# Kernel optimization log

Measured on AMD Instinct MI355X. Metric: run time of the kernel, lower is better.

Reference implementation:

```python
import jax, jax.numpy as jnp
import numpy as np
import math

B, S, D_MODEL, H = 2, 2048, 1024, 16
HD = D_MODEL // H  # head_dim = 64


def _rope(x, seq_len):
    # x: [B, S, H, HD]; standard rotate-half RoPE with base 10000
    d = x.shape[-1]
    inv_freq = 1.0 / (10000.0 ** (jnp.arange(0, d, 2, dtype=jnp.float32) / d))
    t = jnp.arange(seq_len, dtype=jnp.float32)
    freqs = t[:, None] * inv_freq[None, :]              # [S, HD/2]
    emb = jnp.concatenate([freqs, freqs], axis=-1)      # [S, HD]
    cos = jnp.cos(emb)[None, :, None, :]
    sin = jnp.sin(emb)[None, :, None, :]
    x1, x2 = jnp.split(x, 2, axis=-1)
    rot = jnp.concatenate([-x2, x1], axis=-1)
    return x * cos + rot * sin


def setup_inputs() -> dict:
    key = jax.random.key(0)
    ks = jax.random.split(key, 11)
    s = 1.0 / math.sqrt(D_MODEL)
    return {
        "query": jax.random.normal(ks[0], (B, S, D_MODEL), jnp.float32),
        "keys": jax.random.normal(ks[1], (B, S, D_MODEL), jnp.float32),
        "values": jax.random.normal(ks[2], (B, S, D_MODEL), jnp.float32),
        "Wq": jax.random.normal(ks[3], (D_MODEL, D_MODEL), jnp.float32) * s,
        "bq": jnp.zeros((D_MODEL,), jnp.float32),
        "Wk": jax.random.normal(ks[4], (D_MODEL, D_MODEL), jnp.float32) * s,
        "bk": jnp.zeros((D_MODEL,), jnp.float32),
        "Wv": jax.random.normal(ks[5], (D_MODEL, D_MODEL), jnp.float32) * s,
        "bv": jnp.zeros((D_MODEL,), jnp.float32),
        "Wo": jax.random.normal(ks[6], (D_MODEL, D_MODEL), jnp.float32) * s,
        "bo": jnp.zeros((D_MODEL,), jnp.float32),
    }


def reference(query, keys, values, Wq, bq, Wk, bk, Wv, bv, Wo, bo):
    b, s, _ = query.shape
    scale = math.sqrt(HD)
    q = (query @ Wq.T + bq).reshape(b, s, H, HD)   # [B,S,H,HD]
    k = (keys @ Wk.T + bk).reshape(b, s, H, HD)
    v = (values @ Wv.T + bv).reshape(b, s, H, HD)
    q = _rope(q, s)
    k = _rope(k, s)
    # scores: [B,H,Sq,Sk]
    scores = jnp.einsum('bqhd,bkhd->bhqk', q, k)
    causal = jnp.tril(jnp.ones((s, s), dtype=bool))[None, None]
    scores = jnp.where(causal, scores, -jnp.inf) / scale
    attn = jax.nn.softmax(scores, axis=-1)
    ctx = jnp.einsum('bhqk,bkhd->bqhd', attn, v).reshape(b, s, H * HD)
    out = ctx @ Wo.T + bo
    return out, attn
```

## Files before the change

kernel.cpp:

```cpp
#include <hip/hip_runtime.h>
#include <hip/hip_bf16.h>
#include <stdint.h>
#include <math.h>


typedef __attribute__((ext_vector_type(8))) __bf16 bf16x8;
typedef __attribute__((ext_vector_type(4))) float f32x4;

__device__ __forceinline__ unsigned short f2bf(float f) {
  unsigned int u = __float_as_uint(f);
  u += 0x7fffu + ((u >> 16) & 1u);
  return (unsigned short)(u >> 16);
}

typedef const __attribute__((address_space(1))) unsigned int* gas_ptr;
typedef __attribute__((address_space(3))) unsigned int* las_ptr;
__device__ __forceinline__ void glds16(const void* g, void* l) {
  __builtin_amdgcn_global_load_lds((gas_ptr)g, (las_ptr)l, 16, 0, 0);
}

__global__ __launch_bounds__(256) void cvt_all(
    const float* __restrict__ a0, const float* __restrict__ a1,
    const float* __restrict__ a2, const float* __restrict__ w0,
    const float* __restrict__ w1, const float* __restrict__ w2,
    const float* __restrict__ w3, unsigned short* __restrict__ ws,
    float2* __restrict__ rtab) {
  const int z = blockIdx.z;
  if (z == 7) {
    const int i = blockIdx.x * 256 + threadIdx.x;
    if (i < 65536) {
      const int spos = i >> 5, d = i & 31;
      const double invf = pow(10000.0, -(double)d / 32.0);
      double sn, cs;
      sincos((double)spos * invf, &sn, &cs);
      rtab[i] = make_float2((float)cs, (float)sn);
    }
    return;
  }
  const float* src;
  unsigned short* dst;
  int n;
  if (z == 0)      { src = a0; dst = ws;             n = 4194304; }
  else if (z == 1) { src = a1; dst = ws + 4194304;   n = 4194304; }
  else if (z == 2) { src = a2; dst = ws + 8388608;   n = 4194304; }
  else if (z == 3) { src = w0; dst = ws + 12582912;  n = 1048576; }
  else if (z == 4) { src = w1; dst = ws + 13631488;  n = 1048576; }
  else if (z == 5) { src = w2; dst = ws + 14680064;  n = 1048576; }
  else             { src = w3; dst = ws + 15728640;  n = 1048576; }
  const int n4 = n >> 2;
  for (int i = blockIdx.x * 256 + threadIdx.x; i < n4; i += gridDim.x * 256) {
    float4 f = ((const float4*)src)[i];
    ushort4 u;
    u.x = f2bf(f.x); u.y = f2bf(f.y); u.z = f2bf(f.z); u.w = f2bf(f.w);
    ((ushort4*)dst)[i] = u;
  }
}

__global__ __launch_bounds__(256) void gemm_qkv(
    const unsigned short* __restrict__ xq, const unsigned short* __restrict__ xk,
    const unsigned short* __restrict__ xv, const unsigned short* __restrict__ wq,
    const unsigned short* __restrict__ wk, const unsigned short* __restrict__ wv,
    const float* __restrict__ bq, const float* __restrict__ bk,
    const float* __restrict__ bv, const float2* __restrict__ rtab,
    unsigned short* __restrict__ qo, unsigned short* __restrict__ ko,
    unsigned short* __restrict__ vo) {
  const int z = blockIdx.z;
  const unsigned short* A = (z == 0) ? xq : (z == 1) ? xk : xv;
  const unsigned short* W = (z == 0) ? wq : (z == 1) ? wk : wv;
  const float* bias = (z == 0) ? bq : (z == 1) ? bk : bv;
  unsigned short* out = (z == 0) ? qo : (z == 1) ? ko : vo;

  const int t = threadIdx.x;
  const int lane = t & 63, wave = t >> 6;
  const int wr = wave >> 1, wc = wave & 1;
  const int lrow = lane & 15, lkb = lane >> 4;
  const int lin = blockIdx.x + (blockIdx.y << 3);
  const int nl = ((lin & 7) << 5) | (lin >> 3);
  const int m0 = (nl >> 3) * 128, n0 = (nl & 7) * 128;

  __shared__ __align__(16) unsigned short abuf[8192];
  __shared__ __align__(16) unsigned short bbuf[8192];

  f32x4 acc[4][4] = {};

  for (int k0 = 0; k0 < 1024; k0 += 64) {
    __syncthreads();
#pragma unroll
    for (int i = 0; i < 4; ++i) {
      int slot = i * 256 + t;
      int kb = slot >> 7, row = slot & 127;
      glds16(A + (size_t)(m0 + row) * 1024 + k0 + kb * 8, &abuf[slot * 8]);
      glds16(W + (size_t)(n0 + row) * 1024 + k0 + kb * 8, &bbuf[slot * 8]);
    }
    __syncthreads();
#pragma unroll
    for (int ks = 0; ks < 2; ++ks) {
      bf16x8 af[4], bfr[4];
#pragma unroll
      for (int mi = 0; mi < 4; ++mi)
        af[mi] = *(const bf16x8*)&abuf[((ks * 4 + lkb) * 128 + wr * 64 + mi * 16 + lrow) * 8];
#pragma unroll
      for (int ni = 0; ni < 4; ++ni)
        bfr[ni] = *(const bf16x8*)&bbuf[((ks * 4 + lkb) * 128 + wc * 64 + ni * 16 + lrow) * 8];
#pragma unroll
      for (int mi = 0; mi < 4; ++mi)
#pragma unroll
        for (int ni = 0; ni < 4; ++ni)
          acc[mi][ni] = __builtin_amdgcn_mfma_f32_16x16x32_bf16(af[mi], bfr[ni],
                                                                acc[mi][ni], 0, 0, 0);
    }
  }

  const int nbase = n0 + wc * 64;
  float bias_v[4];
#pragma unroll
  for (int ni = 0; ni < 4; ++ni) bias_v[ni] = bias[nbase + ni * 16 + lrow];

  const int mbase = m0 + wr * 64 + 4 * lkb;
  const bool rope = (z < 2);
  const float qsc = (z == 0) ? 0.125f : 1.0f;

#pragma unroll
  for (int mi = 0; mi < 4; ++mi) {
#pragma unroll
    for (int r = 0; r < 4; ++r) {
      const int m = mbase + mi * 16 + r;
      const int bidx = m >> 11, spos = m & 2047;
      float vals[4];
#pragma unroll
      for (int ni = 0; ni < 4; ++ni) vals[ni] = acc[mi][ni][r] + bias_v[ni];
      if (rope) {
#pragma unroll
        for (int ni = 0; ni < 2; ++ni) {
          const int d = ni * 16 + lrow;
          const float2 cs2 = rtab[spos * 32 + d];
          float x1 = vals[ni], x2 = vals[ni + 2];
          vals[ni] = (x1 * cs2.x - x2 * cs2.y) * qsc;
          vals[ni + 2] = (x2 * cs2.x + x1 * cs2.y) * qsc;
        }
      }
#pragma unroll
      for (int ni = 0; ni < 4; ++ni) {
        const int n = nbase + ni * 16 + lrow;
        const int h = n >> 6, d = n & 63;
        out[(size_t)((bidx * 16 + h) * 2048 + spos) * 64 + d] = f2bf(vals[ni]);
      }
    }
  }
}

__global__ __launch_bounds__(256) void gemm_out(
    const unsigned short* __restrict__ A, const unsigned short* __restrict__ W,
    const float* __restrict__ bias, float* __restrict__ out) {
  const int t = threadIdx.x;
  const int lane = t & 63, wave = t >> 6;
  const int wr = wave >> 1, wc = wave & 1;
  const int lrow = lane & 15, lkb = lane >> 4;
  const int lin = blockIdx.x + (blockIdx.y << 3);
  const int nl = ((lin & 7) << 5) | (lin >> 3);
  const int m0 = (nl >> 3) * 128, n0 = (nl & 7) * 128;

  __shared__ __align__(16) unsigned short abuf[8192];
  __shared__ __align__(16) unsigned short bbuf[8192];

  f32x4 acc[4][4] = {};

  for (int k0 = 0; k0 < 1024; k0 += 64) {
    __syncthreads();
#pragma unroll
    for (int i = 0; i < 4; ++i) {
      int slot = i * 256 + t;
      int kb = slot >> 7, row = slot & 127;
      glds16(A + (size_t)(m0 + row) * 1024 + k0 + kb * 8, &abuf[slot * 8]);
      glds16(W + (size_t)(n0 + row) * 1024 + k0 + kb * 8, &bbuf[slot * 8]);
    }
    __syncthreads();
#pragma unroll
    for (int ks = 0; ks < 2; ++ks) {
      bf16x8 af[4], bfr[4];
#pragma unroll
      for (int mi = 0; mi < 4; ++mi)
        af[mi] = *(const bf16x8*)&abuf[((ks * 4 + lkb) * 128 + wr * 64 + mi * 16 + lrow) * 8];
#pragma unroll
      for (int ni = 0; ni < 4; ++ni)
        bfr[ni] = *(const bf16x8*)&bbuf[((ks * 4 + lkb) * 128 + wc * 64 + ni * 16 + lrow) * 8];
#pragma unroll
      for (int mi = 0; mi < 4; ++mi)
#pragma unroll
        for (int ni = 0; ni < 4; ++ni)
          acc[mi][ni] = __builtin_amdgcn_mfma_f32_16x16x32_bf16(af[mi], bfr[ni],
                                                                acc[mi][ni], 0, 0, 0);
    }
  }

  const int nbase = n0 + wc * 64;
  float bias_v[4];
#pragma unroll
  for (int ni = 0; ni < 4; ++ni) bias_v[ni] = bias[nbase + ni * 16 + lrow];
  const int mbase = m0 + wr * 64 + 4 * lkb;
#pragma unroll
  for (int mi = 0; mi < 4; ++mi)
#pragma unroll
    for (int r = 0; r < 4; ++r) {
      const int m = mbase + mi * 16 + r;
      float* orow = out + (size_t)m * 1024 + nbase;
#pragma unroll
      for (int ni = 0; ni < 4; ++ni)
        orow[ni * 16 + lrow] = acc[mi][ni][r] + bias_v[ni];
    }
}

__global__ __launch_bounds__(256) void transpose_v(
    const unsigned short* __restrict__ v, unsigned short* __restrict__ vt) {
  const int s0 = blockIdx.x * 64;
  const int bh = blockIdx.y;
  __shared__ __align__(16) unsigned short tile[64][80];
  const int t = threadIdx.x;
  {
    const int row = t >> 2, cb = t & 3;
    const unsigned short* src = v + (size_t)(bh * 2048 + s0 + row) * 64 + cb * 16;
    *(uint4*)&tile[row][cb * 16] = *(const uint4*)src;
    *(uint4*)&tile[row][cb * 16 + 8] = *(const uint4*)(src + 8);
  }
  __syncthreads();
  {
    const int d = t >> 2, sc = t & 3;
    __align__(16) unsigned short tmp[16];
#pragma unroll
    for (int u = 0; u < 16; ++u) tmp[u] = tile[sc * 16 + u][d];
    unsigned short* dst = vt + (size_t)(bh * 64 + d) * 2048 + s0 + sc * 16;
    *(uint4*)dst = *(const uint4*)&tmp[0];
    *(uint4*)(dst + 8) = *(const uint4*)&tmp[8];
  }
}

__global__ __launch_bounds__(256) void attn_kernel(
    const unsigned short* __restrict__ Q, const unsigned short* __restrict__ Km,
    const unsigned short* __restrict__ Vt, float* __restrict__ attn,
    unsigned short* __restrict__ ctx) {
  const int p = blockIdx.x;
  const int qta = p, qtb = 31 - p;
  const int bh = blockIdx.y;
  const int t = threadIdx.x;
  const int lane = t & 63, wave = t >> 6;
  const int lrow = lane & 15, lg = lane >> 4;
  const int wq0a = qta * 64 + wave * 16;
  const int wq0b = qtb * 64 + wave * 16;

  const unsigned short* Qb = Q + (size_t)bh * 2048 * 64;
  const unsigned short* Kb = Km + (size_t)bh * 2048 * 64;
  const unsigned short* Vb = Vt + (size_t)bh * 64 * 2048;
  float* attn_b = attn + (size_t)bh * 2048 * 2048;

  __shared__ __align__(16) unsigned short kbuf[4096];
  __shared__ __align__(16) unsigned short vbuf[4096];
  __shared__ __align__(16) unsigned short pbuf[4][1024];

  bf16x8 qfa[2], qfb[2];
#pragma unroll
  for (int dk = 0; dk < 2; ++dk) {
    qfa[dk] = *(const bf16x8*)(Qb + (size_t)(wq0a + lrow) * 64 + dk * 32 + lg * 8);
    qfb[dk] = *(const bf16x8*)(Qb + (size_t)(wq0b + lrow) * 64 + dk * 32 + lg * 8);
  }

  float l_a[4] = {0.f, 0.f, 0.f, 0.f};
  float l_b[4] = {0.f, 0.f, 0.f, 0.f};

  auto lupdate = [&](const unsigned short* buf, int kbase, int wq0,
                     const bf16x8* qf, float* l_loc) {
    f32x4 s[4] = {};
#pragma unroll
    for (int fc = 0; fc < 4; ++fc)
#pragma unroll
      for (int dk = 0; dk < 2; ++dk) {
        bf16x8 kf = *(const bf16x8*)&buf[((dk * 4 + lg) * 64 + fc * 16 + lrow) * 8];
        s[fc] = __builtin_amdgcn_mfma_f32_16x16x32_bf16(qf[dk], kf, s[fc], 0, 0, 0);
      }
#pragma unroll
    for (int r = 0; r < 4; ++r) {
      const int qg = wq0 + 4 * lg + r;
      float sum = 0.f;
#pragma unroll
      for (int fc = 0; fc < 4; ++fc) {
        const int kg = kbase + fc * 16 + lrow;
        sum += __expf((kg <= qg) ? s[fc][r] : -1e30f);
      }
      l_loc[r] += sum;
    }
  };

  for (int kt = 0; kt <= qtb; kt += 2) {
    const int k0 = kt * 64;
    const bool two = (kt + 1) <= qtb;
    __syncthreads();
#pragma unroll
    for (int i = 0; i < 2; ++i) {
      int slot = i * 256 + t;
      int cb = slot >> 6, row = slot & 63;
      glds16(Kb + (size_t)(k0 + row) * 64 + cb * 8, &kbuf[slot * 8]);
      if (two)
        glds16(Kb + (size_t)(k0 + 64 + row) * 64 + cb * 8, &vbuf[slot * 8]);
    }
    __syncthreads();
    if (kt <= qta) lupdate(kbuf, k0, wq0a, qfa, l_a);
    lupdate(kbuf, k0, wq0b, qfb, l_b);
    if (two) {
      if (kt + 1 <= qta) lupdate(vbuf, k0 + 64, wq0a, qfa, l_a);
      lupdate(vbuf, k0 + 64, wq0b, qfb, l_b);
    }
  }

  float loglinva[4], loglinvb[4];
#pragma unroll
  for (int r = 0; r < 4; ++r) {
    float la = l_a[r], lb = l_b[r];
#pragma unroll
    for (int off = 1; off < 16; off <<= 1) {
      la += __shfl_xor(la, off);
      lb += __shfl_xor(lb, off);
    }
    loglinva[r] = -__logf(la);
    loglinvb[r] = -__logf(lb);
  }

  f32x4 oaa[4] = {};
  f32x4 oab[4] = {};

  auto process = [&](int k0, int wq0, const bf16x8* qf, const float* loglinv,
                     f32x4* oa) {
    f32x4 s[4] = {};
#pragma unroll
    for (int fc = 0; fc < 4; ++fc)
#pragma unroll
      for (int dk = 0; dk < 2; ++dk) {
        bf16x8 kf = *(const bf16x8*)&kbuf[((dk * 4 + lg) * 64 + fc * 16 + lrow) * 8];
        s[fc] = __builtin_amdgcn_mfma_f32_16x16x32_bf16(qf[dk], kf, s[fc], 0, 0, 0);
      }
#pragma unroll
    for (int r = 0; r < 4; ++r) {
      const int qg = wq0 + 4 * lg + r;
      const int q_ = 4 * lg + r;
      float* arow = attn_b + (size_t)qg * 2048 + k0;
#pragma unroll
      for (int fc = 0; fc < 4; ++fc) {
        const int kg = k0 + fc * 16 + lrow;
        const float pv = (kg <= qg) ? __expf(s[fc][r] + loglinv[r]) : 0.f;
        arow[fc * 16 + lrow] = pv;
        const int k_ = fc * 16 + lrow;
        const int dl = q_ + 16 * ((k_ >> 3) & 3);
        const int kk = k_ >> 5, j = k_ & 7;
        int byteo = (kk * 64 + dl) * 16 + j * 2;
        byteo ^= ((kk * 8 + (dl >> 3)) & 7) << 4;
        *(unsigned short*)((char*)pbuf[wave] + byteo) = f2bf(pv);
      }
    }
#pragma unroll
    for (int kk = 0; kk < 2; ++kk) {
      int rbyte = (kk * 64 + lane) * 16;
      rbyte ^= ((kk * 8 + (lane >> 3)) & 7) << 4;
      bf16x8 pa = *(const bf16x8*)((char*)pbuf[wave] + rbyte);
#pragma unroll
      for (int fd = 0; fd < 4; ++fd) {
        bf16x8 vf = *(const bf16x8*)&vbuf[((kk * 4 + lg) * 64 + fd * 16 + lrow) * 8];
        oa[fd] = __builtin_amdgcn_mfma_f32_16x16x32_bf16(pa, vf, oa[fd], 0, 0, 0);
      }
    }
  };

  for (int kt = 0; kt <= qtb; ++kt) {
    const int k0 = kt * 64;
    __syncthreads();
#pragma unroll
    for (int i = 0; i < 2; ++i) {
      int slot = i * 256 + t;
      int cb = slot >> 6, row = slot & 63;
      glds16(Kb + (size_t)(k0 + row) * 64 + cb * 8, &kbuf[slot * 8]);
      glds16(Vb + (size_t)row * 2048 + k0 + cb * 8, &vbuf[slot * 8]);
    }
    __syncthreads();
    if (kt <= qta) process(k0, wq0a, qfa, loglinva, oaa);
    process(k0, wq0b, qfb, loglinvb, oab);
  }

  {
    const int zc0a = (qta + 1) * 16;
    for (int rr = 0; rr < 16; ++rr) {
      float4* arow = (float4*)(attn_b + (size_t)(wq0a + rr) * 2048);
      for (int c = zc0a + lane; c < 512; c += 64)
        arow[c] = make_float4(0.f, 0.f, 0.f, 0.f);
    }
    const int zc0b = (qtb + 1) * 16;
    for (int rr = 0; rr < 16; ++rr) {
      float4* arow = (float4*)(attn_b + (size_t)(wq0b + rr) * 2048);
      for (int c = zc0b + lane; c < 512; c += 64)
        arow[c] = make_float4(0.f, 0.f, 0.f, 0.f);
    }
  }

  const int bidx = bh >> 4, h = bh & 15;
#pragma unroll
  for (int fd = 0; fd < 4; ++fd)
#pragma unroll
    for (int r = 0; r < 4; ++r) {
      const int qga = wq0a + 4 * lg + r;
      const int qgb = wq0b + 4 * lg + r;
      ctx[(size_t)(bidx * 2048 + qga) * 1024 + h * 64 + fd * 16 + lrow] =
          f2bf(oaa[fd][r]);
      ctx[(size_t)(bidx * 2048 + qgb) * 1024 + h * 64 + fd * 16 + lrow] =
          f2bf(oab[fd][r]);
    }
}

extern "C" void kernel_launch(void* const* d_in, const int* in_sizes, int n_in,
                              void* d_out, int out_size, void* d_ws, size_t ws_size,
                              hipStream_t stream) {
  const float* q_in = (const float*)d_in[0];
  const float* k_in = (const float*)d_in[1];
  const float* v_in = (const float*)d_in[2];
  const float* Wq = (const float*)d_in[3];
  const float* bq = (const float*)d_in[4];
  const float* Wk = (const float*)d_in[5];
  const float* bk = (const float*)d_in[6];
  const float* Wv = (const float*)d_in[7];
  const float* bv = (const float*)d_in[8];
  const float* Wo = (const float*)d_in[9];
  const float* bo = (const float*)d_in[10];

  unsigned short* ws = (unsigned short*)d_ws;
  float* outp = (float*)d_out;

  const size_t OXQ = 0, OXK = 4194304, OXV = 8388608;
  const size_t OWQ = 12582912, OWK = 13631488, OWV = 14680064, OWO = 15728640;
  const size_t OQ = 16777216, OK = 20971520, OV = 25165824;
  const size_t OTAB = 29360128;
  const size_t OVT = OXK;
  const size_t OCTX = OXQ;
  float2* rtab = (float2*)(ws + OTAB);

  cvt_all<<<dim3(512, 1, 8), 256, 0, stream>>>(q_in, k_in, v_in, Wq, Wk, Wv, Wo,
                                               ws, rtab);
  gemm_qkv<<<dim3(8, 32, 3), 256, 0, stream>>>(ws + OXQ, ws + OXK, ws + OXV,
                                               ws + OWQ, ws + OWK, ws + OWV,
                                               bq, bk, bv, rtab,
                                               ws + OQ, ws + OK, ws + OV);
  transpose_v<<<dim3(32, 32), 256, 0, stream>>>(ws + OV, ws + OVT);
  attn_kernel<<<dim3(16, 32), 256, 0, stream>>>(ws + OQ, ws + OK, ws + OVT,
                                                outp + 4194304, ws + OCTX);
  gemm_out<<<dim3(8, 32), 256, 0, stream>>>(ws + OCTX, ws + OWO, bo, outp);
}
```

Baseline: 297.7 us.

## Split paired query tiles across 8 waves instead of serial processing per wave

The attention block grows from 256 to 512 threads. Waves 0-3 now handle the early query tile and waves 4-7 the late tile, where before each wave handled both tiles one after the other. Per-wave work and register pressure drop, and the shared K/V tile loads are spread over twice as many threads. The cost is that the early-tile waves sit idle at barriers during iterations past their causal limit, and the larger block may lower blocks-per-CU occupancy.

```diff
diff --git a/kernel.cpp b/kernel.cpp
--- a/kernel.cpp
+++ b/kernel.cpp
@@ -234,7 +234,7 @@
   }
 }
 
-__global__ __launch_bounds__(256) void attn_kernel(
+__global__ __launch_bounds__(512) void attn_kernel(
     const unsigned short* __restrict__ Q, const unsigned short* __restrict__ Km,
     const unsigned short* __restrict__ Vt, float* __restrict__ attn,
     unsigned short* __restrict__ ctx) {
@@ -243,9 +243,10 @@
   const int bh = blockIdx.y;
   const int t = threadIdx.x;
   const int lane = t & 63, wave = t >> 6;
+  const int wtile = wave >> 2, wid = wave & 3;
   const int lrow = lane & 15, lg = lane >> 4;
-  const int wq0a = qta * 64 + wave * 16;
-  const int wq0b = qtb * 64 + wave * 16;
+  const int myqt = wtile ? qtb : qta;
+  const int wq0 = myqt * 64 + wid * 16;
 
   const unsigned short* Qb = Q + (size_t)bh * 2048 * 64;
   const unsigned short* Kb = Km + (size_t)bh * 2048 * 64;
@@ -254,20 +255,16 @@
 
   __shared__ __align__(16) unsigned short kbuf[4096];
   __shared__ __align__(16) unsigned short vbuf[4096];
-  __shared__ __align__(16) unsigned short pbuf[4][1024];
-
-  bf16x8 qfa[2], qfb[2];
-#pragma unroll
-  for (int dk = 0; dk < 2; ++dk) {
-    qfa[dk] = *(const bf16x8*)(Qb + (size_t)(wq0a + lrow) * 64 + dk * 32 + lg * 8);
-    qfb[dk] = *(const bf16x8*)(Qb + (size_t)(wq0b + lrow) * 64 + dk * 32 + lg * 8);
-  }
-
-  float l_a[4] = {0.f, 0.f, 0.f, 0.f};
-  float l_b[4] = {0.f, 0.f, 0.f, 0.f};
-
-  auto lupdate = [&](const unsigned short* buf, int kbase, int wq0,
-                     const bf16x8* qf, float* l_loc) {
+  __shared__ __align__(16) unsigned short pbuf[8][1024];
+
+  bf16x8 qf[2];
+#pragma unroll
+  for (int dk = 0; dk < 2; ++dk)
+    qf[dk] = *(const bf16x8*)(Qb + (size_t)(wq0 + lrow) * 64 + dk * 32 + lg * 8);
+
+  float l_loc[4] = {0.f, 0.f, 0.f, 0.f};
+
+  auto lupdate = [&](const unsigned short* buf, int kbase) {
     f32x4 s[4] = {};
 #pragma unroll
     for (int fc = 0; fc < 4; ++fc)
@@ -293,41 +290,38 @@
     const int k0 = kt * 64;
     const bool two = (kt + 1) <= qtb;
     __syncthreads();
-#pragma unroll
-    for (int i = 0; i < 2; ++i) {
-      int slot = i * 256 + t;
-      int cb = slot >> 6, row = slot & 63;
-      glds16(Kb + (size_t)(k0 + row) * 64 + cb * 8, &kbuf[slot * 8]);
+    {
+      int cb = t >> 6, row = t & 63;
+      glds16(Kb + (size_t)(k0 + row) * 64 + cb * 8, &kbuf[t * 8]);
       if (two)
-        glds16(Kb + (size_t)(k0 + 64 + row) * 64 + cb * 8, &vbuf[slot * 8]);
-    }
-    __syncthreads();
-    if (kt <= qta) lupdate(kbuf, k0, wq0a, qfa, l_a);
-    lupdate(kbuf, k0, wq0b, qfb, l_b);
-    if (two) {
-      if (kt + 1 <= qta) lupdate(vbuf, k0 + 64, wq0a, qfa, l_a);
-      lupdate(vbuf, k0 + 64, wq0b, qfb, l_b);
-    }
-  }
-
-  float loglinva[4], loglinvb[4];
+        glds16(Kb + (size_t)(k0 + 64 + row) * 64 + cb * 8, &vbuf[t * 8]);
+    }
+    __syncthreads();
+    if (kt <= myqt) lupdate(kbuf, k0);
+    if (two && (kt + 1) <= myqt) lupdate(vbuf, k0 + 64);
+  }
+
+  float loglinv[4];
 #pragma unroll
   for (int r = 0; r < 4; ++r) {
-    float la = l_a[r], lb = l_b[r];
-#pragma unroll
-    for (int off = 1; off < 16; off <<= 1) {
-      la += __shfl_xor(la, off);
-      lb += __shfl_xor(lb, off);
-    }
-    loglinva[r] = -__logf(la);
-    loglinvb[r] = -__logf(lb);
-  }
-
-  f32x4 oaa[4] = {};
-  f32x4 oab[4] = {};
-
-  auto process = [&](int k0, int wq0, const bf16x8* qf, const float* loglinv,
-                     f32x4* oa) {
+    float l = l_loc[r];
+#pragma unroll
+    for (int off = 1; off < 16; off <<= 1) l += __shfl_xor(l, off);
+    loglinv[r] = -__logf(l);
+  }
+
+  f32x4 oa[4] = {};
+
+  for (int kt = 0; kt <= qtb; ++kt) {
+    const int k0 = kt * 64;
+    __syncthreads();
+    {
+      int cb = t >> 6, row = t & 63;
+      glds16(Kb + (size_t)(k0 + row) * 64 + cb * 8, &kbuf[t * 8]);
+      glds16(Vb + (size_t)row * 2048 + k0 + cb * 8, &vbuf[t * 8]);
+    }
+    __syncthreads();
+    if (kt > myqt) continue;
     f32x4 s[4] = {};
 #pragma unroll
     for (int fc = 0; fc < 4; ++fc)
@@ -365,36 +359,15 @@
         oa[fd] = __builtin_amdgcn_mfma_f32_16x16x32_bf16(pa, vf, oa[fd], 0, 0, 0);
       }
     }
-  };
-
-  for (int kt = 0; kt <= qtb; ++kt) {
-    const int k0 = kt * 64;
-    __syncthreads();
-#pragma unroll
-    for (int i = 0; i < 2; ++i) {
-      int slot = i * 256 + t;
-      int cb = slot >> 6, row = slot & 63;
-      glds16(Kb + (size_t)(k0 + row) * 64 + cb * 8, &kbuf[slot * 8]);
-      glds16(Vb + (size_t)row * 2048 + k0 + cb * 8, &vbuf[slot * 8]);
-    }
-    __syncthreads();
-    if (kt <= qta) process(k0, wq0a, qfa, loglinva, oaa);
-    process(k0, wq0b, qfb, loglinvb, oab);
   }
 
   {
-    const int zc0a = (qta + 1) * 16;
+    const int zc0 = (myqt + 1) * 16;
     for (int rr = 0; rr < 16; ++rr) {
-      float4* arow = (float4*)(attn_b + (size_t)(wq0a + rr) * 2048);
-      for (int c = zc0a + lane; c < 512; c += 64)
+      float4* arow = (float4*)(attn_b + (size_t)(wq0 + rr) * 2048);
+      for (int c = zc0 + lane; c < 512; c += 64)
         arow[c] = make_float4(0.f, 0.f, 0.f, 0.f);
     }
-    const int zc0b = (qtb + 1) * 16;
-    for (int rr = 0; rr < 16; ++rr) {
-      float4* arow = (float4*)(attn_b + (size_t)(wq0b + rr) * 2048);
-      for (int c = zc0b + lane; c < 512; c += 64)
-        arow[c] = make_float4(0.f, 0.f, 0.f, 0.f);
-    }
   }
 
   const int bidx = bh >> 4, h = bh & 15;
@@ -402,12 +375,9 @@
   for (int fd = 0; fd < 4; ++fd)
 #pragma unroll
     for (int r = 0; r < 4; ++r) {
-      const int qga = wq0a + 4 * lg + r;
-      const int qgb = wq0b + 4 * lg + r;
-      ctx[(size_t)(bidx * 2048 + qga) * 1024 + h * 64 + fd * 16 + lrow] =
-          f2bf(oaa[fd][r]);
-      ctx[(size_t)(bidx * 2048 + qgb) * 1024 + h * 64 + fd * 16 + lrow] =
-          f2bf(oab[fd][r]);
+      const int qg = wq0 + 4 * lg + r;
+      ctx[(size_t)(bidx * 2048 + qg) * 1024 + h * 64 + fd * 16 + lrow] =
+          f2bf(oa[fd][r]);
     }
 }
 
@@ -444,7 +414,7 @@
                                                bq, bk, bv, rtab,
                                                ws + OQ, ws + OK, ws + OV);
   transpose_v<<<dim3(32, 32), 256, 0, stream>>>(ws + OV, ws + OVT);
-  attn_kernel<<<dim3(16, 32), 256, 0, stream>>>(ws + OQ, ws + OK, ws + OVT,
+  attn_kernel<<<dim3(16, 32), 512, 0, stream>>>(ws + OQ, ws + OK, ws + OVT,
                                                 outp + 4194304, ws + OCTX);
   gemm_out<<<dim3(8, 32), 256, 0, stream>>>(ws + OCTX, ws + OWO, bo, outp);
 }
```

Measured after the change: 293.0 us (median of 2 runs). About the same (-1.6%).
